# Kernel tuning notes

Hardware: AMD Instinct MI355X
Metric: run time of the kernel (lower is better)

## Reference

```python
import jax, jax.numpy as jnp
import numpy as np

B, T, E, D = 8, 4096, 64, 8  # batch, seq, embed_dim, head_dim (embed_dim//heads)


def setup_inputs() -> dict:
    key = jax.random.key(0)
    ks = jax.random.split(key, 7)
    scale = 1.0 / np.sqrt(E).astype(np.float32)
    return {
        "x": jax.random.normal(ks[0], (B, T, E), dtype=jnp.float32),
        "Wq": jax.random.normal(ks[1], (E, D), dtype=jnp.float32) * scale,
        "bq": jax.random.normal(ks[2], (D,), dtype=jnp.float32) * 0.01,
        "Wk": jax.random.normal(ks[3], (E, D), dtype=jnp.float32) * scale,
        "bk": jax.random.normal(ks[4], (D,), dtype=jnp.float32) * 0.01,
        "Wv": jax.random.normal(ks[5], (E, D), dtype=jnp.float32) * scale,
        "bv": jax.random.normal(ks[6], (D,), dtype=jnp.float32) * 0.01,
    }


def reference(x, Wq, bq, Wk, bk, Wv, bv):
    # q, k, v: [B, T, D]
    q = x @ Wq + bq
    k = x @ Wk + bk
    v = x @ Wv + bv
    b, t, d = k.shape
    # FAITHFUL to source: key(x).view(B, C, T) is a RESHAPE, not a transpose.
    w = q @ k.reshape(b, d, t)  # [B, T, T]
    # tril then masked_fill(w == 0, -inf): zero entries (incl. masked-out
    # upper triangle) become -inf before softmax.
    w = jnp.tril(w)
    w = jnp.where(w == 0, -jnp.inf, w)
    w = jax.nn.softmax(w / np.float32(np.sqrt(d)), axis=-1)
    return w @ v  # [B, T, D]
```

## Files before the change

### kernel.cpp

```cpp
#include <hip/hip_runtime.h>
#include <math.h>

#define BB 8
#define TT 4096
#define EE 64
#define DD 8
#define QSCALE 0.51012604f
#define CSHIFT -12.0f

typedef _Float16 half8  __attribute__((ext_vector_type(8)));
typedef _Float16 half4v __attribute__((ext_vector_type(4)));
typedef float    floatx4 __attribute__((ext_vector_type(4)));

__global__ __launch_bounds__(256) void proj_kernel(
    const float* __restrict__ x,
    const float* __restrict__ Wq, const float* __restrict__ bq,
    const float* __restrict__ Wk, const float* __restrict__ bk,
    const float* __restrict__ Wv, const float* __restrict__ bv,
    _Float16* __restrict__ qh, _Float16* __restrict__ ks, _Float16* __restrict__ vT)
{
    __shared__ float    xs[32][EE + 1];
    __shared__ _Float16 qsm[256];
    __shared__ _Float16 ksm[256];
    __shared__ _Float16 vsm[256];

    const int tid   = threadIdx.x;
    const int blk   = blockIdx.x;
    const int b     = blk >> 7;
    const int tbase = (blk & 127) << 2;

#pragma unroll
    for (int m2 = 0; m2 < 2; ++m2) {
        int r = (tid >> 4) + (m2 << 4);
        int c = (tid & 15) << 2;
        int t = ((r >> 2) << 9) + tbase + (r & 3);
        float4 a = *(const float4*)(x + (size_t)(b * TT + t) * EE + c);
        xs[r][c+0] = a.x; xs[r][c+1] = a.y; xs[r][c+2] = a.z; xs[r][c+3] = a.w;
    }
    __syncthreads();

    const int r = tid >> 3;
    const int d = tid & 7;
    float accq = bq[d], acck = bk[d], accv = bv[d];
#pragma unroll
    for (int e = 0; e < EE; ++e) {
        float xv = xs[r][e];
        accq = fmaf(xv, Wq[e*DD + d], accq);
        acck = fmaf(xv, Wk[e*DD + d], acck);
        accv = fmaf(xv, Wv[e*DD + d], accv);
    }
    qsm[tid] = (_Float16)(accq * QSCALE);
    ksm[((r & 3) << 6) + (d << 3) + (r >> 2)] = (_Float16)acck;
    vsm[(d << 5) + r] = (_Float16)accv;
    __syncthreads();

    if (tid < 32) {
        half8 qv = *(half8*)(qsm + tid * 8);
        *(half8*)(qh + (size_t)b*(TT*DD) + (size_t)(tid >> 2)*(512*DD)
                     + (size_t)tbase*DD + ((tid & 3) << 3)) = qv;
        half8 kv = *(half8*)(ksm + tid * 8);
        *(half8*)(ks + (size_t)b*(TT*DD) + (size_t)tbase*64 + tid * 8) = kv;
    } else if (tid >= 64 && tid < 128) {
        int idx = tid - 64, d2 = idx >> 3, g2 = idx & 7;
        half4v vv = *(half4v*)(vsm + (d2 << 5) + (g2 << 2));
        *(half4v*)(vT + (size_t)b*(16*TT) + (size_t)d2*TT + (g2 << 9) + tbase) = vv;
    } else if (tid >= 128 && tid < 136) {
        int g2 = tid - 128;
        half4v ones = {(_Float16)1.0f, (_Float16)1.0f, (_Float16)1.0f, (_Float16)1.0f};
        *(half4v*)(vT + (size_t)b*(16*TT) + (size_t)8*TT + (g2 << 9) + tbase) = ones;
    }
}

__global__ __launch_bounds__(512, 6) void attn_kernel(
    const _Float16* __restrict__ qh, const _Float16* __restrict__ ks,
    const _Float16* __restrict__ vT, float* __restrict__ out)
{
    __shared__ floatx4 obuf[2][8][64];

    const int lane = threadIdx.x & 63;
    const int wave = threadIdx.x >> 6;
    const int g = lane >> 4;
    const int n = lane & 15;

    const int blk = blockIdx.x;
    const int bb  = blk >> 7;
    const int p   = blk & 127;
    const int ntA = (p >> 2) + 1;
    const int ntB = ((255 - p) >> 2) + 1;
    const int total = ntA + ntB;
    const int r0A = p << 4;
    const int r0B = (255 - p) << 4;

    const _Float16* ksb = ks + (size_t)bb * (TT*DD);
    const _Float16* vTb = vT + (size_t)bb * (16*TT);

    half8 qfA, qfB;
    {
        half8 z;
#pragma unroll
        for (int j = 0; j < 8; ++j) z[j] = (_Float16)0.0f;
        qfA = z; qfB = z;
        if (g == 0) {
            qfA = *(const half8*)(qh + ((size_t)bb*TT + r0A + n) * DD);
            qfB = *(const half8*)(qh + ((size_t)bb*TT + r0B + n) * DD);
        }
    }

    floatx4 oA = {0.f, 0.f, 0.f, 0.f};
    floatx4 oB = {0.f, 0.f, 0.f, 0.f};
    const floatx4 C12 = {CSHIFT, CSHIFT, CSHIFT, CSHIFT};

    const int  srcA  = ((g & 1) << 5) | n;
    const int  srcB  = srcA + 16;
    const bool hiSub = (g & 2) != 0;

    for (int i = wave; i < total; i += 8) {
        const bool isA = i < ntA;
        const int  tt  = isA ? i : (i - ntA);
        const int  r0w = isA ? r0A : r0B;
        half8 qf; if (isA) qf = qfA; else qf = qfB;
        const int t2base = tt << 6;

        floatx4 S[4];
#pragma unroll
        for (int s = 0; s < 4; ++s) {
            half8 ka = *(const half8*)(ksb + (size_t)(t2base + (s << 4) + n) * DD);
            S[s] = __builtin_amdgcn_mfma_f32_16x16x32_f16(ka, qf, C12, 0, 0, 0);
        }

        if (t2base + 63 > r0w) {
            const int lim = r0w + n - t2base - (g << 2);
#pragma unroll
            for (int s = 0; s < 4; ++s)
#pragma unroll
                for (int rr = 0; rr < 4; ++rr)
                    if ((s << 4) + rr > lim) S[s][rr] = -INFINITY;
        }

        int lo[4], hi[4];
#pragma unroll
        for (int s = 0; s < 4; ++s) {
            float p0 = (S[s][0] == CSHIFT) ? 0.f : __builtin_amdgcn_exp2f(S[s][0]);
            float p1 = (S[s][1] == CSHIFT) ? 0.f : __builtin_amdgcn_exp2f(S[s][1]);
            float p2 = (S[s][2] == CSHIFT) ? 0.f : __builtin_amdgcn_exp2f(S[s][2]);
            float p3 = (S[s][3] == CSHIFT) ? 0.f : __builtin_amdgcn_exp2f(S[s][3]);
            lo[s] = __builtin_bit_cast(int, __builtin_amdgcn_cvt_pkrtz(p0, p1));
            hi[s] = __builtin_bit_cast(int, __builtin_amdgcn_cvt_pkrtz(p2, p3));
        }

        floatx4 o;
        if (isA) o = oA; else o = oB;
#pragma unroll
        for (int pv = 0; pv < 2; ++pv) {
            const int sA = pv << 1, sB = sA | 1;
            int a0 = __shfl(lo[sA], srcA, 64), b0 = __shfl(lo[sB], srcA, 64);
            int a1 = __shfl(hi[sA], srcA, 64), b1 = __shfl(hi[sB], srcA, 64);
            int a2 = __shfl(lo[sA], srcB, 64), b2 = __shfl(lo[sB], srcB, 64);
            int a3 = __shfl(hi[sA], srcB, 64), b3 = __shfl(hi[sB], srcB, 64);
            int4 wi;
            wi.x = hiSub ? b0 : a0;
            wi.y = hiSub ? b1 : a1;
            wi.z = hiSub ? b2 : a2;
            wi.w = hiSub ? b3 : a3;
            half8 pb = __builtin_bit_cast(half8, wi);
            half8 va = *(const half8*)(vTb + (size_t)n * TT + t2base + (pv << 5) + (g << 3));
            o = __builtin_amdgcn_mfma_f32_16x16x32_f16(va, pb, o, 0, 0, 0);
        }
        if (isA) oA = o; else oB = o;
    }

    obuf[0][wave][lane] = oA;
    obuf[1][wave][lane] = oB;
    __syncthreads();

    if (wave < 2) {
        floatx4 osum = {0.f, 0.f, 0.f, 0.f};
#pragma unroll
        for (int w = 0; w < 8; ++w) osum += obuf[wave][w][lane];
        const float l    = __shfl(osum[0], 32 + n, 64);
        const float linv = 1.0f / l;
        const int   r0   = wave ? r0B : r0A;
        if (g < 2) {
            float4 res;
            res.x = osum[0] * linv; res.y = osum[1] * linv;
            res.z = osum[2] * linv; res.w = osum[3] * linv;
            *(float4*)(out + (((size_t)bb * TT + r0 + n) * DD) + (g << 2)) = res;
        }
    }
}

extern "C" void kernel_launch(void* const* d_in, const int* in_sizes, int n_in,
                              void* d_out, int out_size, void* d_ws, size_t ws_size,
                              hipStream_t stream) {
    const float* x  = (const float*)d_in[0];
    const float* Wq = (const float*)d_in[1];
    const float* bq = (const float*)d_in[2];
    const float* Wk = (const float*)d_in[3];
    const float* bk = (const float*)d_in[4];
    const float* Wv = (const float*)d_in[5];
    const float* bv = (const float*)d_in[6];
    float* out = (float*)d_out;

    _Float16* qhp = (_Float16*)d_ws;
    _Float16* ksp = qhp + (size_t)BB * TT * DD;
    _Float16* vTp = ksp + (size_t)BB * TT * DD;

    proj_kernel<<<BB * TT / 32, 256, 0, stream>>>(x, Wq, bq, Wk, bk, Wv, bv, qhp, ksp, vTp);
    attn_kernel<<<1024, 512, 0, stream>>>(qhp, ksp, vTp, out);
}
```

Baseline: 102.5 us.

## Prefetch next K tile, split A/B attention loops, drop zero-score check

```diff
diff --git a/kernel.cpp b/kernel.cpp
--- a/kernel.cpp
+++ b/kernel.cpp
@@ -71,7 +71,7 @@
     }
 }
 
-__global__ __launch_bounds__(512, 6) void attn_kernel(
+__global__ __launch_bounds__(512, 8) void attn_kernel(
     const _Float16* __restrict__ qh, const _Float16* __restrict__ ks,
     const _Float16* __restrict__ vT, float* __restrict__ out)
 {
@@ -87,12 +87,12 @@
     const int p   = blk & 127;
     const int ntA = (p >> 2) + 1;
     const int ntB = ((255 - p) >> 2) + 1;
-    const int total = ntA + ntB;
     const int r0A = p << 4;
     const int r0B = (255 - p) << 4;
 
     const _Float16* ksb = ks + (size_t)bb * (TT*DD);
     const _Float16* vTb = vT + (size_t)bb * (16*TT);
+    const _Float16* vrow = vTb + (size_t)n * TT + (g << 3);
 
     half8 qfA, qfB;
     {
@@ -114,60 +114,73 @@
     const int  srcB  = srcA + 16;
     const bool hiSub = (g & 2) != 0;
 
-    for (int i = wave; i < total; i += 8) {
-        const bool isA = i < ntA;
-        const int  tt  = isA ? i : (i - ntA);
-        const int  r0w = isA ? r0A : r0B;
-        half8 qf; if (isA) qf = qfA; else qf = qfB;
-        const int t2base = tt << 6;
-
-        floatx4 S[4];
-#pragma unroll
-        for (int s = 0; s < 4; ++s) {
-            half8 ka = *(const half8*)(ksb + (size_t)(t2base + (s << 4) + n) * DD);
-            S[s] = __builtin_amdgcn_mfma_f32_16x16x32_f16(ka, qf, C12, 0, 0, 0);
-        }
-
-        if (t2base + 63 > r0w) {
-            const int lim = r0w + n - t2base - (g << 2);
-#pragma unroll
-            for (int s = 0; s < 4; ++s)
-#pragma unroll
-                for (int rr = 0; rr < 4; ++rr)
-                    if ((s << 4) + rr > lim) S[s][rr] = -INFINITY;
-        }
-
-        int lo[4], hi[4];
-#pragma unroll
-        for (int s = 0; s < 4; ++s) {
-            float p0 = (S[s][0] == CSHIFT) ? 0.f : __builtin_amdgcn_exp2f(S[s][0]);
-            float p1 = (S[s][1] == CSHIFT) ? 0.f : __builtin_amdgcn_exp2f(S[s][1]);
-            float p2 = (S[s][2] == CSHIFT) ? 0.f : __builtin_amdgcn_exp2f(S[s][2]);
-            float p3 = (S[s][3] == CSHIFT) ? 0.f : __builtin_amdgcn_exp2f(S[s][3]);
-            lo[s] = __builtin_bit_cast(int, __builtin_amdgcn_cvt_pkrtz(p0, p1));
-            hi[s] = __builtin_bit_cast(int, __builtin_amdgcn_cvt_pkrtz(p2, p3));
-        }
-
-        floatx4 o;
-        if (isA) o = oA; else o = oB;
-#pragma unroll
-        for (int pv = 0; pv < 2; ++pv) {
-            const int sA = pv << 1, sB = sA | 1;
-            int a0 = __shfl(lo[sA], srcA, 64), b0 = __shfl(lo[sB], srcA, 64);
-            int a1 = __shfl(hi[sA], srcA, 64), b1 = __shfl(hi[sB], srcA, 64);
-            int a2 = __shfl(lo[sA], srcB, 64), b2 = __shfl(lo[sB], srcB, 64);
-            int a3 = __shfl(hi[sA], srcB, 64), b3 = __shfl(hi[sB], srcB, 64);
-            int4 wi;
-            wi.x = hiSub ? b0 : a0;
-            wi.y = hiSub ? b1 : a1;
-            wi.z = hiSub ? b2 : a2;
-            wi.w = hiSub ? b3 : a3;
-            half8 pb = __builtin_bit_cast(half8, wi);
-            half8 va = *(const half8*)(vTb + (size_t)n * TT + t2base + (pv << 5) + (g << 3));
-            o = __builtin_amdgcn_mfma_f32_16x16x32_f16(va, pb, o, 0, 0, 0);
-        }
-        if (isA) oA = o; else oB = o;
-    }
+#define ATTN_LOOP(NT, R0, QF, OACC)                                             \
+    {                                                                           \
+        int i = wave;                                                           \
+        half8 ck0, ck1, ck2, ck3;                                               \
+        if (i < (NT)) {                                                         \
+            const _Float16* kp = ksb + (size_t)(i << 6) * DD + (size_t)n * DD;  \
+            ck0 = *(const half8*)(kp);                                          \
+            ck1 = *(const half8*)(kp + 16 * DD);                                \
+            ck2 = *(const half8*)(kp + 32 * DD);                                \
+            ck3 = *(const half8*)(kp + 48 * DD);                                \
+        }                                                                       \
+        for (; i < (NT); i += 8) {                                              \
+            const int t2base = i << 6;                                          \
+            int inx = i + 8; if (inx >= (NT)) inx = i;                          \
+            const _Float16* kpn = ksb + (size_t)(inx << 6) * DD + (size_t)n * DD;\
+            half8 nk0 = *(const half8*)(kpn);                                   \
+            half8 nk1 = *(const half8*)(kpn + 16 * DD);                         \
+            half8 nk2 = *(const half8*)(kpn + 32 * DD);                         \
+            half8 nk3 = *(const half8*)(kpn + 48 * DD);                         \
+            half8 va0 = *(const half8*)(vrow + t2base);                         \
+            half8 va1 = *(const half8*)(vrow + t2base + 32);                    \
+            floatx4 S[4];                                                       \
+            S[0] = __builtin_amdgcn_mfma_f32_16x16x32_f16(ck0, QF, C12, 0, 0, 0);\
+            S[1] = __builtin_amdgcn_mfma_f32_16x16x32_f16(ck1, QF, C12, 0, 0, 0);\
+            S[2] = __builtin_amdgcn_mfma_f32_16x16x32_f16(ck2, QF, C12, 0, 0, 0);\
+            S[3] = __builtin_amdgcn_mfma_f32_16x16x32_f16(ck3, QF, C12, 0, 0, 0);\
+            if (t2base + 63 > (R0)) {                                           \
+                const int lim = (R0) + n - t2base - (g << 2);                   \
+                _Pragma("unroll")                                               \
+                for (int s = 0; s < 4; ++s)                                     \
+                    _Pragma("unroll")                                           \
+                    for (int rr = 0; rr < 4; ++rr)                              \
+                        if ((s << 4) + rr > lim) S[s][rr] = -INFINITY;          \
+            }                                                                   \
+            int lo[4], hi[4];                                                   \
+            _Pragma("unroll")                                                   \
+            for (int s = 0; s < 4; ++s) {                                       \
+                float p0 = __builtin_amdgcn_exp2f(S[s][0]);                     \
+                float p1 = __builtin_amdgcn_exp2f(S[s][1]);                     \
+                float p2 = __builtin_amdgcn_exp2f(S[s][2]);                     \
+                float p3 = __builtin_amdgcn_exp2f(S[s][3]);                     \
+                lo[s] = __builtin_bit_cast(int, __builtin_amdgcn_cvt_pkrtz(p0, p1));\
+                hi[s] = __builtin_bit_cast(int, __builtin_amdgcn_cvt_pkrtz(p2, p3));\
+            }                                                                   \
+            _Pragma("unroll")                                                   \
+            for (int pv = 0; pv < 2; ++pv) {                                    \
+                const int sA2 = pv << 1, sB2 = sA2 | 1;                         \
+                int a0 = __shfl(lo[sA2], srcA, 64), b0 = __shfl(lo[sB2], srcA, 64);\
+                int a1 = __shfl(hi[sA2], srcA, 64), b1 = __shfl(hi[sB2], srcA, 64);\
+                int a2 = __shfl(lo[sA2], srcB, 64), b2 = __shfl(lo[sB2], srcB, 64);\
+                int a3 = __shfl(hi[sA2], srcB, 64), b3 = __shfl(hi[sB2], srcB, 64);\
+                int4 wi;                                                        \
+                wi.x = hiSub ? b0 : a0;                                         \
+                wi.y = hiSub ? b1 : a1;                                         \
+                wi.z = hiSub ? b2 : a2;                                         \
+                wi.w = hiSub ? b3 : a3;                                         \
+                half8 pb = __builtin_bit_cast(half8, wi);                       \
+                half8 vv = pv ? va1 : va0;                                      \
+                OACC = __builtin_amdgcn_mfma_f32_16x16x32_f16(vv, pb, OACC, 0, 0, 0);\
+            }                                                                   \
+            ck0 = nk0; ck1 = nk1; ck2 = nk2; ck3 = nk3;                         \
+        }                                                                       \
+    }
+
+    ATTN_LOOP(ntA, r0A, qfA, oA)
+    ATTN_LOOP(ntB, r0B, qfB, oB)
+#undef ATTN_LOOP
 
     obuf[0][wave][lane] = oA;
     obuf[1][wave][lane] = oB;
```

Measured after the change: 116.8 us. 1.14x slower.
